# Kernel optimization log

Measured on AMD Instinct MI355X. Metric: run time of the kernel, lower is better.

## Reference

```python
import jax, jax.numpy as jnp
import numpy as np

H = 1024
E = 8
TOP_K = 2
B, S = 4, 2048


def setup_inputs() -> dict:
    key = jax.random.key(0)
    ks = jax.random.split(key, 8)
    scale = 0.02
    return {
        "x": jax.random.normal(ks[0], (B, S, H), dtype=jnp.float32),
        "router_w": jax.random.normal(ks[1], (H, E), dtype=jnp.float32) * scale,
        "router_b": jnp.zeros((E,), dtype=jnp.float32),
        "w1": jax.random.normal(ks[2], (E, H, 4 * H), dtype=jnp.float32) * scale,
        "b1": jnp.zeros((E, 4 * H), dtype=jnp.float32),
        "w2": jax.random.normal(ks[3], (E, 4 * H, H), dtype=jnp.float32) * scale,
        "b2": jnp.zeros((E, H), dtype=jnp.float32),
    }


def reference(x, router_w, router_b, w1, b1, w2, b2):
    b, s, h = x.shape
    n_exp = w1.shape[0]
    x_flat = x.reshape(-1, h)  # [T, H]
    T = x_flat.shape[0]

    # Router: softmax then top-k, renormalize top-k probs (matches torch code).
    logits = x_flat @ router_w + router_b            # [T, E]
    probs = jax.nn.softmax(logits, axis=-1)
    top_values, top_indices = jax.lax.top_k(probs, TOP_K)  # [T, k]
    top_values = top_values / jnp.sum(top_values, axis=-1, keepdims=True)

    # Per-token combine weight for each expert (0 if token not routed there).
    combine = jnp.zeros((T, n_exp), dtype=x.dtype)
    combine = combine.at[jnp.arange(T)[:, None], top_indices].add(top_values)  # [T, E]

    # Loop over the small fixed expert set; masked combine weights zero out
    # contributions from unrouted tokens, matching the gather/scatter original.
    out = jnp.zeros_like(x_flat)
    for e in range(n_exp):
        hmid = jax.nn.gelu(x_flat @ w1[e] + b1[e], approximate=False)  # [T, 4H]
        y = hmid @ w2[e] + b2[e]                                       # [T, H]
        out = out + combine[:, e:e + 1] * y
    return out.reshape(b, s, h)
```

## Files before the change

kernel.cpp:

```cpp
#include <hip/hip_runtime.h>
#include <hip/hip_bf16.h>
#include <math.h>

#define TT 8192
#define HD 1024
#define FHD 4096
#define NE 8
#define NTMAX 136
#define NWG1 4352

typedef short s16x8 __attribute__((ext_vector_type(8)));
typedef float f32x4 __attribute__((ext_vector_type(4)));
using bf16 = __hip_bfloat16;
typedef unsigned int u32;

#define OFF_COUNTS 0
#define OFF_DONE   32
#define OFF_CURSOR 64
#define OFF_OFFS   128
#define OFF_E0     256
#define OFF_E1     (OFF_E0 + 4*TT)
#define OFF_W0     (OFF_E1 + 4*TT)
#define OFF_W1     (OFF_W0 + 4*TT)
#define OFF_S0     (OFF_W1 + 4*TT)
#define OFF_S1     (OFF_S0 + 4*TT)
#define OFF_TID    (OFF_S1 + 4*TT)
#define OFF_TW     (OFF_TID + 8*TT)
#define OFF_TMR    (OFF_TW + 8*TT)
#define OFF_TME    (OFF_TMR + 4*144)
#define OFF_TMN    (OFF_TME + 4*144)
#define OFF_XBF    (OFF_TMN + 64)
#define OFF_W1T    (OFF_XBF + 2*TT*HD)
#define OFF_W2T    (OFF_W1T + 2*NE*HD*FHD)
#define OFF_HMID   (OFF_W2T + 2*NE*HD*FHD)
#define OFF_YS     (OFF_HMID + (size_t)2*(2*TT)*FHD)

__device__ __forceinline__ void gload_lds16(const void* g, void* l) {
    __builtin_amdgcn_global_load_lds(
        (const __attribute__((address_space(1))) u32*)g,
        (__attribute__((address_space(3))) u32*)l, 16, 0, 0);
}

__device__ __forceinline__ void transpose_panel(const float* __restrict__ in,
        bf16* __restrict__ out, int R, int C, int rem, int tid, char* smem) {
    float (*tile)[65]  = reinterpret_cast<float(*)[65]>(smem);
    bf16  (*btile)[264] = reinterpret_cast<bf16(*)[264]>(smem + 16640);
    int kch = R >> 8, nch = C >> 6;
    int per = kch * nch;
    int e = rem / per;
    int rem2 = rem % per;
    int kc = rem2 / nch, nc = rem2 % nch;
    int k0 = kc << 8, n0 = nc << 6;
    const float* ine = in + (size_t)e * R * C;
    bf16* oute = out + (size_t)e * R * C;
    for (int s = 0; s < 4; ++s) {
        int ks = k0 + s * 64;
#pragma unroll
        for (int i = 0; i < 4; ++i) {
            int lin = tid + i * 256;
            int r = lin >> 4, cg = lin & 15;
            float4 v = *reinterpret_cast<const float4*>(&ine[(size_t)(ks + r) * C + n0 + cg * 4]);
            tile[r][cg * 4 + 0] = v.x; tile[r][cg * 4 + 1] = v.y;
            tile[r][cg * 4 + 2] = v.z; tile[r][cg * 4 + 3] = v.w;
        }
        __syncthreads();
#pragma unroll
        for (int i = 0; i < 4; ++i) {
            int lin = tid + i * 256;
            int n = lin >> 4, kg = lin & 15;
            bf16 h[4];
            h[0] = __float2bfloat16(tile[kg * 4 + 0][n]);
            h[1] = __float2bfloat16(tile[kg * 4 + 1][n]);
            h[2] = __float2bfloat16(tile[kg * 4 + 2][n]);
            h[3] = __float2bfloat16(tile[kg * 4 + 3][n]);
            *reinterpret_cast<uint2*>(&btile[n][s * 64 + kg * 4]) = *reinterpret_cast<uint2*>(h);
        }
        __syncthreads();
    }
#pragma unroll
    for (int i = 0; i < 8; ++i) {
        int lin = tid + i * 256;
        int n = lin >> 5, kk = lin & 31;
        *reinterpret_cast<uint4*>(&oute[(size_t)(n0 + n) * R + k0 + kk * 8]) =
            *reinterpret_cast<const uint4*>(&btile[n][kk * 8]);
    }
}

__global__ __launch_bounds__(256) void fused1_kernel(
        const float* __restrict__ x, const float* __restrict__ rw, const float* __restrict__ rb,
        const float* __restrict__ w1, bf16* __restrict__ xbf, bf16* __restrict__ w1t,
        int* __restrict__ e0a, int* __restrict__ e1a,
        float* __restrict__ w0a, float* __restrict__ w1a,
        int* __restrict__ counts, int* __restrict__ done,
        int* __restrict__ offs, int* __restrict__ cursor,
        int* __restrict__ tmr, int* __restrict__ tme, int* __restrict__ tmn) {
    __shared__ __attribute__((aligned(16))) char smem[50432];
    int bid = blockIdx.x;
    int tid = threadIdx.x;
    if (bid < 2048) {
        transpose_panel(w1, w1t, HD, FHD, bid, tid, smem);
        return;
    }
    int rbid = bid - 2048;
    int wid = tid >> 6, lane = tid & 63;
    int t = rbid * 4 + wid;
    const float* xp = x + (size_t)t * HD + lane * 16;
    float xv[16];
#pragma unroll
    for (int j = 0; j < 4; ++j) {
        float4 v = *reinterpret_cast<const float4*>(&xp[j * 4]);
        xv[4 * j] = v.x; xv[4 * j + 1] = v.y; xv[4 * j + 2] = v.z; xv[4 * j + 3] = v.w;
    }
    {
        bf16 hv[16];
#pragma unroll
        for (int j = 0; j < 16; ++j) hv[j] = __float2bfloat16(xv[j]);
        uint4* dst = reinterpret_cast<uint4*>(&xbf[(size_t)t * HD + lane * 16]);
        dst[0] = reinterpret_cast<uint4*>(hv)[0];
        dst[1] = reinterpret_cast<uint4*>(hv)[1];
    }
    float acc[8] = {0.f, 0.f, 0.f, 0.f, 0.f, 0.f, 0.f, 0.f};
    const float* rp = rw + (size_t)(lane * 16) * NE;
#pragma unroll
    for (int hh = 0; hh < 16; ++hh) {
        float4 r0 = *reinterpret_cast<const float4*>(&rp[hh * 8]);
        float4 r1 = *reinterpret_cast<const float4*>(&rp[hh * 8 + 4]);
        acc[0] += xv[hh] * r0.x; acc[1] += xv[hh] * r0.y;
        acc[2] += xv[hh] * r0.z; acc[3] += xv[hh] * r0.w;
        acc[4] += xv[hh] * r1.x; acc[5] += xv[hh] * r1.y;
        acc[6] += xv[hh] * r1.z; acc[7] += xv[hh] * r1.w;
    }
#pragma unroll
    for (int e = 0; e < 8; ++e) {
#pragma unroll
        for (int off = 32; off > 0; off >>= 1) acc[e] += __shfl_xor(acc[e], off, 64);
    }
    if (lane == 0) {
        float lg[8];
#pragma unroll
        for (int e = 0; e < 8; ++e) lg[e] = acc[e] + rb[e];
        int a = 0;
#pragma unroll
        for (int e = 1; e < 8; ++e) if (lg[e] > lg[a]) a = e;
        int b = (a == 0) ? 1 : 0;
#pragma unroll
        for (int e = 0; e < 8; ++e) if (e != a && e != b && lg[e] > lg[b]) b = e;
        float wa = 1.0f / (1.0f + expf(lg[b] - lg[a]));
        float wb = 1.0f / (1.0f + expf(lg[a] - lg[b]));
        e0a[t] = a; e1a[t] = b; w0a[t] = wa; w1a[t] = wb;
        atomicAdd(&counts[a], 1);
        atomicAdd(&counts[b], 1);
    }
    __syncthreads();
    __shared__ int lastFlag;
    if (tid == 0) {
        __threadfence();
        lastFlag = (atomicAdd(done, 1) == 2047) ? 1 : 0;
    }
    __syncthreads();
    if (!lastFlag) return;
    __threadfence();
    __shared__ int cbase[NE + 1], tbase[NE + 1];
    if (tid == 0) {
        int s = 0, ntt = 0;
        for (int e = 0; e < NE; ++e) {
            int c = atomicAdd(&counts[e], 0);
            cbase[e] = s; tbase[e] = ntt;
            s += c; ntt += (c + 127) >> 7;
        }
        cbase[NE] = s; tbase[NE] = ntt;
        tmn[0] = ntt;
        offs[NE] = s;
    }
    __syncthreads();
    if (tid < NE) { offs[tid] = cbase[tid]; cursor[tid] = cbase[tid]; }
    if (tid < NTMAX) {
        int ntt = tbase[NE];
        if (tid < ntt) {
            int e = 0;
            while (tbase[e + 1] <= tid) ++e;
            tmr[tid] = cbase[e] + ((tid - tbase[e]) << 7);
            tme[tid] = e;
        } else { tmr[tid] = 0; tme[tid] = 0; }
    }
}

__global__ __launch_bounds__(256) void scatter_kernel(const int* __restrict__ e0a, const int* __restrict__ e1a,
        const float* __restrict__ w0a, const float* __restrict__ w1a,
        int* __restrict__ cursor, int* __restrict__ tid_arr, float* __restrict__ tw_arr,
        int* __restrict__ slot0, int* __restrict__ slot1) {
    int t = blockIdx.x * 256 + threadIdx.x;
    int s0 = atomicAdd(&cursor[e0a[t]], 1);
    tid_arr[s0] = t; tw_arr[s0] = w0a[t]; slot0[t] = s0;
    int s1 = atomicAdd(&cursor[e1a[t]], 1);
    tid_arr[s1] = t; tw_arr[s1] = w1a[t]; slot1[t] = s1;
}

__global__ __launch_bounds__(256) void fused2_kernel(
        const float* __restrict__ w2, bf16* __restrict__ w2t,
        const bf16* __restrict__ xbf, const bf16* __restrict__ w1t,
        const float* __restrict__ b1, const int* __restrict__ offs,
        const int* __restrict__ tid_arr, bf16* __restrict__ hmid,
        const int* __restrict__ tmr, const int* __restrict__ tme, const int* __restrict__ tmn) {
    __shared__ __attribute__((aligned(16))) char smem[50432];
    int bid = blockIdx.x;
    int tid = threadIdx.x;
    if (bid < 2048) {
        transpose_panel(w2, w2t, FHD, HD, bid, tid, smem);
        return;
    }
    bf16* As = reinterpret_cast<bf16*>(smem);
    bf16* Bs = reinterpret_cast<bf16*>(smem + 8192);
    int*  toks = reinterpret_cast<int*>(smem + 16384);
    int orig = bid - 2048;
    int wg = (orig & 7) * (NWG1 >> 3) + (orig >> 3);
    int st = wg / 136, within = wg % 136;
    int tidx = (st >> 2) * 17 + (within % 17);
    int nt = (st & 3) * 8 + (within / 17);
    if (tidx >= tmn[0]) return;
    int e = tme[tidx];
    int row0 = tmr[tidx];
    int s1 = offs[e + 1];
    int n0 = nt * 128;
    if (tid < 128) { int s = row0 + tid; toks[tid] = tid_arr[(s < s1) ? s : (s1 - 1)]; }
    __syncthreads();
    int lane = tid & 63, w = tid >> 6;
    int wrow = (w >> 1) * 64, wcol = (w & 1) * 64;
    int lr = lane & 15, lk = (lane >> 4) * 8;
    int srow = lane >> 2, seg = lane & 3;
    int tokA0 = toks[w * 32 + srow];
    int tokA1 = toks[w * 32 + 16 + srow];
    const bf16* w1e = w1t + (size_t)e * FHD * HD;
    const bf16* bsrc0 = w1e + (size_t)(n0 + w * 32 + srow) * HD + seg * 8;
    const bf16* bsrc1 = w1e + (size_t)(n0 + w * 32 + 16 + srow) * HD + seg * 8;
    const bf16* asrc0 = xbf + (size_t)tokA0 * HD + seg * 8;
    const bf16* asrc1 = xbf + (size_t)tokA1 * HD + seg * 8;
    bf16* aDst0 = &As[(w * 32) * 32];
    bf16* aDst1 = &As[(w * 32 + 16) * 32];
    bf16* bDst0 = &Bs[(w * 32) * 32];
    bf16* bDst1 = &Bs[(w * 32 + 16) * 32];
    f32x4 acc[4][4] = {};
    for (int k0 = 0; k0 < HD; k0 += 32) {
        gload_lds16(asrc0 + k0, aDst0);
        gload_lds16(asrc1 + k0, aDst1);
        gload_lds16(bsrc0 + k0, bDst0);
        gload_lds16(bsrc1 + k0, bDst1);
        __syncthreads();
        s16x8 aF[4], bF[4];
#pragma unroll
        for (int m = 0; m < 4; ++m) aF[m] = *reinterpret_cast<const s16x8*>(&As[(wrow + m * 16 + lr) * 32 + lk]);
#pragma unroll
        for (int n = 0; n < 4; ++n) bF[n] = *reinterpret_cast<const s16x8*>(&Bs[(wcol + n * 16 + lr) * 32 + lk]);
#pragma unroll
        for (int m = 0; m < 4; ++m)
#pragma unroll
            for (int n = 0; n < 4; ++n)
                acc[m][n] = __builtin_amdgcn_mfma_f32_16x16x32_bf16(aF[m], bF[n], acc[m][n], 0, 0, 0);
        __syncthreads();
    }
#pragma unroll
    for (int m = 0; m < 4; ++m) {
#pragma unroll
        for (int n = 0; n < 4; ++n) {
            int col = n0 + wcol + n * 16 + lr;
            float bv = b1[(size_t)e * FHD + col];
#pragma unroll
            for (int r = 0; r < 4; ++r) {
                int row = wrow + m * 16 + (lane >> 4) * 4 + r;
                int slot = row0 + row;
                if (slot < s1) {
                    float v2 = acc[m][n][r] + bv;
                    v2 = 0.5f * v2 * (1.0f + erff(v2 * 0.70710678118f));
                    hmid[(size_t)slot * FHD + col] = __float2bfloat16(v2);
                }
            }
        }
    }
}

__global__ __launch_bounds__(256) void gemm2_kernel(const bf16* __restrict__ hmid, const bf16* __restrict__ w2t,
        const float* __restrict__ b2, const int* __restrict__ offs, float* __restrict__ ys,
        const int* __restrict__ tmr, const int* __restrict__ tme, const int* __restrict__ tmn) {
    __shared__ bf16 As[128 * 32];
    __shared__ bf16 Bs[128 * 32];
    int nwg = gridDim.x;
    int orig = blockIdx.x;
    int wg = (orig & 7) * (nwg >> 3) + (orig >> 3);
    int st = wg / 68, within = wg % 68;
    int tidx = (st >> 1) * 17 + (within % 17);
    int nt = (st & 1) * 4 + (within / 17);
    if (tidx >= tmn[0]) return;
    int e = tme[tidx];
    int row0 = tmr[tidx];
    int s1 = offs[e + 1];
    int n0 = nt * 128;
    int tid = threadIdx.x;
    int lane = tid & 63, w = tid >> 6;
    int wrow = (w >> 1) * 64, wcol = (w & 1) * 64;
    int lr = lane & 15, lk = (lane >> 4) * 8;
    int srow = lane >> 2, seg = lane & 3;
    int ar0 = row0 + w * 32 + srow;      if (ar0 >= s1) ar0 = s1 - 1;
    int ar1 = row0 + w * 32 + 16 + srow; if (ar1 >= s1) ar1 = s1 - 1;
    const bf16* w2e = w2t + (size_t)e * HD * FHD;
    const bf16* bsrc0 = w2e + (size_t)(n0 + w * 32 + srow) * FHD + seg * 8;
    const bf16* bsrc1 = w2e + (size_t)(n0 + w * 32 + 16 + srow) * FHD + seg * 8;
    const bf16* asrc0 = hmid + (size_t)ar0 * FHD + seg * 8;
    const bf16* asrc1 = hmid + (size_t)ar1 * FHD + seg * 8;
    bf16* aDst0 = &As[(w * 32) * 32];
    bf16* aDst1 = &As[(w * 32 + 16) * 32];
    bf16* bDst0 = &Bs[(w * 32) * 32];
    bf16* bDst1 = &Bs[(w * 32 + 16) * 32];
    f32x4 acc[4][4] = {};
    for (int k0 = 0; k0 < FHD; k0 += 32) {
        gload_lds16(asrc0 + k0, aDst0);
        gload_lds16(asrc1 + k0, aDst1);
        gload_lds16(bsrc0 + k0, bDst0);
        gload_lds16(bsrc1 + k0, bDst1);
        __syncthreads();
        s16x8 aF[4], bF[4];
#pragma unroll
        for (int m = 0; m < 4; ++m) aF[m] = *reinterpret_cast<const s16x8*>(&As[(wrow + m * 16 + lr) * 32 + lk]);
#pragma unroll
        for (int n = 0; n < 4; ++n) bF[n] = *reinterpret_cast<const s16x8*>(&Bs[(wcol + n * 16 + lr) * 32 + lk]);
#pragma unroll
        for (int m = 0; m < 4; ++m)
#pragma unroll
            for (int n = 0; n < 4; ++n)
                acc[m][n] = __builtin_amdgcn_mfma_f32_16x16x32_bf16(aF[m], bF[n], acc[m][n], 0, 0, 0);
        __syncthreads();
    }
#pragma unroll
    for (int m = 0; m < 4; ++m) {
#pragma unroll
        for (int n = 0; n < 4; ++n) {
            int col = n0 + wcol + n * 16 + lr;
            float bv = b2[(size_t)e * HD + col];
#pragma unroll
            for (int r = 0; r < 4; ++r) {
                int row = wrow + m * 16 + (lane >> 4) * 4 + r;
                int slot = row0 + row;
                if (slot < s1) ys[(size_t)slot * HD + col] = acc[m][n][r] + bv;
            }
        }
    }
}

__global__ __launch_bounds__(256) void combine_kernel(const float* __restrict__ ys,
        const int* __restrict__ slot0, const int* __restrict__ slot1,
        const float* __restrict__ tw, float* __restrict__ out) {
    int t = blockIdx.x;
    int c = threadIdx.x * 4;
    int sa = slot0[t], sb = slot1[t];
    float wa = tw[sa], wb = tw[sb];
    float4 a = *reinterpret_cast<const float4*>(&ys[(size_t)sa * HD + c]);
    float4 b = *reinterpret_cast<const float4*>(&ys[(size_t)sb * HD + c]);
    float4 o;
    o.x = wa * a.x + wb * b.x; o.y = wa * a.y + wb * b.y;
    o.z = wa * a.z + wb * b.z; o.w = wa * a.w + wb * b.w;
    *reinterpret_cast<float4*>(&out[(size_t)t * HD + c]) = o;
}

extern "C" void kernel_launch(void* const* d_in, const int* in_sizes, int n_in,
                              void* d_out, int out_size, void* d_ws, size_t ws_size,
                              hipStream_t stream) {
    const float* x  = (const float*)d_in[0];
    const float* rw = (const float*)d_in[1];
    const float* rb = (const float*)d_in[2];
    const float* w1 = (const float*)d_in[3];
    const float* b1 = (const float*)d_in[4];
    const float* w2 = (const float*)d_in[5];
    const float* b2 = (const float*)d_in[6];
    float* out = (float*)d_out;
    char* ws = (char*)d_ws;

    int*   counts  = (int*)(ws + OFF_COUNTS);
    int*   done    = (int*)(ws + OFF_DONE);
    int*   cursor  = (int*)(ws + OFF_CURSOR);
    int*   offs    = (int*)(ws + OFF_OFFS);
    int*   e0a     = (int*)(ws + OFF_E0);
    int*   e1a     = (int*)(ws + OFF_E1);
    float* w0a     = (float*)(ws + OFF_W0);
    float* w1a     = (float*)(ws + OFF_W1);
    int*   slot0   = (int*)(ws + OFF_S0);
    int*   slot1   = (int*)(ws + OFF_S1);
    int*   tid_arr = (int*)(ws + OFF_TID);
    float* tw_arr  = (float*)(ws + OFF_TW);
    int*   tmr     = (int*)(ws + OFF_TMR);
    int*   tme     = (int*)(ws + OFF_TME);
    int*   tmn     = (int*)(ws + OFF_TMN);
    bf16*  xbf     = (bf16*)(ws + OFF_XBF);
    bf16*  w1t     = (bf16*)(ws + OFF_W1T);
    bf16*  w2t     = (bf16*)(ws + OFF_W2T);
    bf16*  hmid    = (bf16*)(ws + OFF_HMID);
    float* ys      = (float*)(ws + OFF_YS);

    hipMemsetAsync(counts, 0, 64, stream);

    fused1_kernel<<<4096, 256, 0, stream>>>(x, rw, rb, w1, xbf, w1t,
        e0a, e1a, w0a, w1a, counts, done, offs, cursor, tmr, tme, tmn);
    scatter_kernel<<<TT / 256, 256, 0, stream>>>(e0a, e1a, w0a, w1a, cursor,
        tid_arr, tw_arr, slot0, slot1);
    fused2_kernel<<<2048 + NWG1, 256, 0, stream>>>(w2, w2t, xbf, w1t, b1, offs,
        tid_arr, hmid, tmr, tme, tmn);
    gemm2_kernel<<<(HD / 128) * NTMAX, 256, 0, stream>>>(hmid, w2t, b2, offs, ys, tmr, tme, tmn);
    combine_kernel<<<TT, 256, 0, stream>>>(ys, slot0, slot1, tw_arr, out);
}
```

Measured before the change: 880.8 us.

## Double K-tile depth to 64 with XOR-swizzled LDS layout in both expert GEMMs

Both grouped GEMM kernels now stage a 64-wide K slice per iteration instead of 32. This halves the number of barrier pairs and global-to-LDS rounds per tile. The LDS rows use an XOR swizzle on 16-byte octets to avoid bank conflicts on fragment reads, and s_setprio is raised around the MFMA block. The trade-off is double the LDS footprint (the smem offsets move), which may reduce occupancy.

```diff
diff --git a/kernel.cpp b/kernel.cpp
--- a/kernel.cpp
+++ b/kernel.cpp
@@ -210,8 +210,8 @@
         return;
     }
     bf16* As = reinterpret_cast<bf16*>(smem);
-    bf16* Bs = reinterpret_cast<bf16*>(smem + 8192);
-    int*  toks = reinterpret_cast<int*>(smem + 16384);
+    bf16* Bs = reinterpret_cast<bf16*>(smem + 16384);
+    int*  toks = reinterpret_cast<int*>(smem + 32768);
     int orig = bid - 2048;
     int wg = (orig & 7) * (NWG1 >> 3) + (orig >> 3);
     int st = wg / 136, within = wg % 136;
@@ -226,36 +226,47 @@
     __syncthreads();
     int lane = tid & 63, w = tid >> 6;
     int wrow = (w >> 1) * 64, wcol = (w & 1) * 64;
-    int lr = lane & 15, lk = (lane >> 4) * 8;
-    int srow = lane >> 2, seg = lane & 3;
-    int tokA0 = toks[w * 32 + srow];
-    int tokA1 = toks[w * 32 + 16 + srow];
+    int lr = lane & 15, kg = lane >> 4;
+    int srow = tid >> 3, oct = tid & 7;
+    int socts = (oct ^ (srow & 7)) * 8;
     const bf16* w1e = w1t + (size_t)e * FHD * HD;
-    const bf16* bsrc0 = w1e + (size_t)(n0 + w * 32 + srow) * HD + seg * 8;
-    const bf16* bsrc1 = w1e + (size_t)(n0 + w * 32 + 16 + srow) * HD + seg * 8;
-    const bf16* asrc0 = xbf + (size_t)tokA0 * HD + seg * 8;
-    const bf16* asrc1 = xbf + (size_t)tokA1 * HD + seg * 8;
-    bf16* aDst0 = &As[(w * 32) * 32];
-    bf16* aDst1 = &As[(w * 32 + 16) * 32];
-    bf16* bDst0 = &Bs[(w * 32) * 32];
-    bf16* bDst1 = &Bs[(w * 32 + 16) * 32];
+    const bf16* pA[4]; const bf16* pB[4];
+#pragma unroll
+    for (int i = 0; i < 4; ++i) {
+        int r = i * 32 + srow;
+        pA[i] = xbf + (size_t)toks[r] * HD + socts;
+        pB[i] = w1e + (size_t)(n0 + r) * HD + socts;
+    }
+    int ldst = tid * 8;
+    int koff0 = (kg * 8) ^ ((lr & 7) << 3);
+    int koff1 = (32 + kg * 8) ^ ((lr & 7) << 3);
     f32x4 acc[4][4] = {};
-    for (int k0 = 0; k0 < HD; k0 += 32) {
-        gload_lds16(asrc0 + k0, aDst0);
-        gload_lds16(asrc1 + k0, aDst1);
-        gload_lds16(bsrc0 + k0, bDst0);
-        gload_lds16(bsrc1 + k0, bDst1);
-        __syncthreads();
-        s16x8 aF[4], bF[4];
-#pragma unroll
-        for (int m = 0; m < 4; ++m) aF[m] = *reinterpret_cast<const s16x8*>(&As[(wrow + m * 16 + lr) * 32 + lk]);
-#pragma unroll
-        for (int n = 0; n < 4; ++n) bF[n] = *reinterpret_cast<const s16x8*>(&Bs[(wcol + n * 16 + lr) * 32 + lk]);
+    for (int k0 = 0; k0 < HD; k0 += 64) {
+#pragma unroll
+        for (int i = 0; i < 4; ++i) {
+            gload_lds16(pA[i] + k0, &As[i * 2048 + ldst]);
+            gload_lds16(pB[i] + k0, &Bs[i * 2048 + ldst]);
+        }
+        __syncthreads();
+        s16x8 aF[4][2], bF[4][2];
+#pragma unroll
+        for (int m = 0; m < 4; ++m) {
+            int rowA = wrow + m * 16 + lr;
+            int rowB = wcol + m * 16 + lr;
+            aF[m][0] = *reinterpret_cast<const s16x8*>(&As[rowA * 64 + koff0]);
+            aF[m][1] = *reinterpret_cast<const s16x8*>(&As[rowA * 64 + koff1]);
+            bF[m][0] = *reinterpret_cast<const s16x8*>(&Bs[rowB * 64 + koff0]);
+            bF[m][1] = *reinterpret_cast<const s16x8*>(&Bs[rowB * 64 + koff1]);
+        }
+        __builtin_amdgcn_s_setprio(1);
 #pragma unroll
         for (int m = 0; m < 4; ++m)
 #pragma unroll
             for (int n = 0; n < 4; ++n)
-                acc[m][n] = __builtin_amdgcn_mfma_f32_16x16x32_bf16(aF[m], bF[n], acc[m][n], 0, 0, 0);
+#pragma unroll
+                for (int s = 0; s < 2; ++s)
+                    acc[m][n] = __builtin_amdgcn_mfma_f32_16x16x32_bf16(aF[m][s], bF[n][s], acc[m][n], 0, 0, 0);
+        __builtin_amdgcn_s_setprio(0);
         __syncthreads();
     }
 #pragma unroll
@@ -266,7 +277,7 @@
             float bv = b1[(size_t)e * FHD + col];
 #pragma unroll
             for (int r = 0; r < 4; ++r) {
-                int row = wrow + m * 16 + (lane >> 4) * 4 + r;
+                int row = wrow + m * 16 + kg * 4 + r;
                 int slot = row0 + row;
                 if (slot < s1) {
                     float v2 = acc[m][n][r] + bv;
@@ -281,8 +292,8 @@
 __global__ __launch_bounds__(256) void gemm2_kernel(const bf16* __restrict__ hmid, const bf16* __restrict__ w2t,
         const float* __restrict__ b2, const int* __restrict__ offs, float* __restrict__ ys,
         const int* __restrict__ tmr, const int* __restrict__ tme, const int* __restrict__ tmn) {
-    __shared__ bf16 As[128 * 32];
-    __shared__ bf16 Bs[128 * 32];
+    __shared__ bf16 As[128 * 64];
+    __shared__ bf16 Bs[128 * 64];
     int nwg = gridDim.x;
     int orig = blockIdx.x;
     int wg = (orig & 7) * (nwg >> 3) + (orig >> 3);
@@ -297,36 +308,48 @@
     int tid = threadIdx.x;
     int lane = tid & 63, w = tid >> 6;
     int wrow = (w >> 1) * 64, wcol = (w & 1) * 64;
-    int lr = lane & 15, lk = (lane >> 4) * 8;
-    int srow = lane >> 2, seg = lane & 3;
-    int ar0 = row0 + w * 32 + srow;      if (ar0 >= s1) ar0 = s1 - 1;
-    int ar1 = row0 + w * 32 + 16 + srow; if (ar1 >= s1) ar1 = s1 - 1;
+    int lr = lane & 15, kg = lane >> 4;
+    int srow = tid >> 3, oct = tid & 7;
+    int socts = (oct ^ (srow & 7)) * 8;
     const bf16* w2e = w2t + (size_t)e * HD * FHD;
-    const bf16* bsrc0 = w2e + (size_t)(n0 + w * 32 + srow) * FHD + seg * 8;
-    const bf16* bsrc1 = w2e + (size_t)(n0 + w * 32 + 16 + srow) * FHD + seg * 8;
-    const bf16* asrc0 = hmid + (size_t)ar0 * FHD + seg * 8;
-    const bf16* asrc1 = hmid + (size_t)ar1 * FHD + seg * 8;
-    bf16* aDst0 = &As[(w * 32) * 32];
-    bf16* aDst1 = &As[(w * 32 + 16) * 32];
-    bf16* bDst0 = &Bs[(w * 32) * 32];
-    bf16* bDst1 = &Bs[(w * 32 + 16) * 32];
+    const bf16* pA[4]; const bf16* pB[4];
+#pragma unroll
+    for (int i = 0; i < 4; ++i) {
+        int r = i * 32 + srow;
+        int ar = row0 + r; if (ar >= s1) ar = s1 - 1;
+        pA[i] = hmid + (size_t)ar * FHD + socts;
+        pB[i] = w2e + (size_t)(n0 + r) * FHD + socts;
+    }
+    int ldst = tid * 8;
+    int koff0 = (kg * 8) ^ ((lr & 7) << 3);
+    int koff1 = (32 + kg * 8) ^ ((lr & 7) << 3);
     f32x4 acc[4][4] = {};
-    for (int k0 = 0; k0 < FHD; k0 += 32) {
-        gload_lds16(asrc0 + k0, aDst0);
-        gload_lds16(asrc1 + k0, aDst1);
-        gload_lds16(bsrc0 + k0, bDst0);
-        gload_lds16(bsrc1 + k0, bDst1);
-        __syncthreads();
-        s16x8 aF[4], bF[4];
-#pragma unroll
-        for (int m = 0; m < 4; ++m) aF[m] = *reinterpret_cast<const s16x8*>(&As[(wrow + m * 16 + lr) * 32 + lk]);
-#pragma unroll
-        for (int n = 0; n < 4; ++n) bF[n] = *reinterpret_cast<const s16x8*>(&Bs[(wcol + n * 16 + lr) * 32 + lk]);
+    for (int k0 = 0; k0 < FHD; k0 += 64) {
+#pragma unroll
+        for (int i = 0; i < 4; ++i) {
+            gload_lds16(pA[i] + k0, &As[i * 2048 + ldst]);
+            gload_lds16(pB[i] + k0, &Bs[i * 2048 + ldst]);
+        }
+        __syncthreads();
+        s16x8 aF[4][2], bF[4][2];
+#pragma unroll
+        for (int m = 0; m < 4; ++m) {
+            int rowA = wrow + m * 16 + lr;
+            int rowB = wcol + m * 16 + lr;
+            aF[m][0] = *reinterpret_cast<const s16x8*>(&As[rowA * 64 + koff0]);
+            aF[m][1] = *reinterpret_cast<const s16x8*>(&As[rowA * 64 + koff1]);
+            bF[m][0] = *reinterpret_cast<const s16x8*>(&Bs[rowB * 64 + koff0]);
+            bF[m][1] = *reinterpret_cast<const s16x8*>(&Bs[rowB * 64 + koff1]);
+        }
+        __builtin_amdgcn_s_setprio(1);
 #pragma unroll
         for (int m = 0; m < 4; ++m)
 #pragma unroll
             for (int n = 0; n < 4; ++n)
-                acc[m][n] = __builtin_amdgcn_mfma_f32_16x16x32_bf16(aF[m], bF[n], acc[m][n], 0, 0, 0);
+#pragma unroll
+                for (int s = 0; s < 2; ++s)
+                    acc[m][n] = __builtin_amdgcn_mfma_f32_16x16x32_bf16(aF[m][s], bF[n][s], acc[m][n], 0, 0, 0);
+        __builtin_amdgcn_s_setprio(0);
         __syncthreads();
     }
 #pragma unroll
@@ -337,7 +360,7 @@
             float bv = b2[(size_t)e * HD + col];
 #pragma unroll
             for (int r = 0; r < 4; ++r) {
-                int row = wrow + m * 16 + (lane >> 4) * 4 + r;
+                int row = wrow + m * 16 + kg * 4 + r;
                 int slot = row0 + row;
                 if (slot < s1) ys[(size_t)slot * HD + col] = acc[m][n][r] + bv;
             }
```

Result: slower. 956.3 us (+8.6%).
